# Kernel tuning notes

Measured on AMD Instinct MI355X. Metric: run time of the kernel, lower is better.

## Reference

```python
import jax, jax.numpy as jnp
import numpy as np

B, T, C = 4, 1024, 512      # batch, seq_len, n_attn
H, TT, D = 1, 1024, 16      # n_head (forced to 1 by kv.view), ctx_len, head_size


def setup_inputs() -> dict:
    key = jax.random.key(0)
    ks = jax.random.split(key, 13)
    s = 0.02
    return {
        "x": jax.random.normal(ks[0], (B, T, C), jnp.float32),
        "time_w": 1.0 + 0.1 * jax.random.normal(ks[1], (H, TT), jnp.float32),
        "time_alpha": 1.0 + 0.1 * jax.random.normal(ks[2], (H, 1, TT), jnp.float32),
        "time_beta": 1.0 + 0.1 * jax.random.normal(ks[3], (H, TT, 1), jnp.float32),
        "time_gamma": 1.0 + 0.1 * jax.random.normal(ks[4], (TT, 1), jnp.float32),
        "Wk": s * jax.random.normal(ks[5], (D, C), jnp.float32),
        "bk": jnp.zeros((D,), jnp.float32),
        "Wv": s * jax.random.normal(ks[6], (D, C), jnp.float32),
        "bv": jnp.zeros((D,), jnp.float32),
        "Wr": s * jax.random.normal(ks[7], (D, C), jnp.float32),
        "br": jnp.zeros((D,), jnp.float32),
        "Wo": s * jax.random.normal(ks[8], (64, D), jnp.float32),
        "bo": jnp.zeros((64,), jnp.float32),
    }


def reference(x, time_w, time_alpha, time_beta, time_gamma,
              Wk, bk, Wv, bv, Wr, br, Wo, bo):
    Tq = x.shape[1]
    # --- Toeplitz decay-matrix build (pad / tile / reshape trick) ---
    w = jnp.pad(time_w, ((0, 0), (0, TT)))                    # [H, 2TT]
    w = jnp.tile(w, (1, TT))[:, :-TT]                         # [H, 2TT*TT - TT]
    w = w.reshape(-1, TT, 2 * TT - 1)[:, :, TT - 1:]          # [H, TT, TT]
    w = w[:, :Tq, :Tq] * time_alpha[:, :, :Tq] * time_beta[:, :Tq, :]  # [H, T, T]
    # --- time shift on first half of channels (ZeroPad2d((0,0,1,-1))) ---
    half = x.shape[-1] // 2
    xs = jnp.pad(x[:, :, :half], ((0, 0), (1, 0), (0, 0)))[:, :-1]   # shift right by 1
    xx = jnp.concatenate([xs, x[:, :, half:]], axis=-1)              # [B, T, C]
    # --- k / v / r projections ---
    k = jnp.exp(jnp.clip(xx @ Wk.T + bk, -60.0, 30.0))        # [B, T, D]
    v = xx @ Wv.T + bv                                        # [B, T, D]
    r = xx @ Wr.T + br                                        # [B, T, D]
    sum_k = jnp.cumsum(k, axis=1)                             # [B, T, D]
    kv = k * v                                                # [B, T, D]
    # torch: kv.view(B,T,1,D).transpose(1,2) -> [B,1,T,D]; einsum 'htu,bthd->bhud'
    # broadcasts w's h=1 against kv's time axis and kv's t=1 against w's t axis:
    #   wkv[b,h,u,d] = (sum_t w[0,t,u]) * kv[b,h(time),d]
    w_sum = jnp.sum(w, axis=1)[0]                             # [T] over u
    wkv_full = w_sum[None, None, :, None] * kv[:, :, None, :] # [B, T, T, D]
    wkv = jnp.mean(wkv_full, axis=1)                          # mean over h -> [B, T, D]
    rwkv = r * wkv / (sum_k + 1e-8)                           # [B, T, D]
    out = (rwkv @ Wo.T + bo) * time_gamma[:Tq, :]             # [B, T, 64]
    return out
```

## Files before the change

### kernel.cpp

```cpp
#include <hip/hip_runtime.h>
#include <hip/hip_bf16.h>

typedef __hip_bfloat16 bf16;


__device__ __forceinline__ float ldf(const void* p, int f, long idx) {
    if (f == 0) return ((const float*)p)[idx];
    if (f == 1) {
        unsigned int u = ((unsigned int)((const unsigned short*)p)[idx]) << 16;
        float r; __builtin_memcpy(&r, &u, 4); return r;
    }
    return 0.f;
}

__device__ __forceinline__ int sniff_one(const unsigned short* u, int els) {
    int n16 = els < 64 ? els : 64;
    bool allzero = true;
    for (int j = 0; j < n16; ++j) if (u[j] != 0) { allzero = false; break; }
    if (allzero) return 2;
    int npair = n16 / 2;
    for (int j = 0; j < npair; ++j) {
        unsigned short lo = u[2 * j], hi = u[2 * j + 1];
        int elo = (lo >> 7) & 0xFF, ehi = (hi >> 7) & 0xFF;
        bool lo_ok = (elo >= 64 && elo <= 190) || lo == 0;
        bool hi_ok = (ehi >= 64 && ehi <= 190) || hi == 0;
        if (!(lo_ok && hi_ok)) return 0;
    }
    return 1;
}

__global__ __launch_bounds__(256) void setup_kernel(
    const void* x, const void* tw, const void* alpha, const void* beta,
    const void* gamma, const void* Wk, const void* bk, const void* Wv,
    const void* bv, const void* Wr, const void* br, const void* Wo,
    const void* bo,
    int n0, int n1, int n2, int n3, int n4, int n5, int n6, int n7,
    int n8, int n9, int n10, int n11, int n12,
    int* __restrict__ flags,
    float* __restrict__ WT4, float* __restrict__ biasWS,
    float* __restrict__ WoF, float* __restrict__ boF,
    float* __restrict__ gammaF, float* __restrict__ segzero,
    float* __restrict__ w_sum)
{
    __shared__ int sf[16];
    __shared__ float red[256];
    int tid = threadIdx.x;
    const void* ps[13] = {x,tw,alpha,beta,gamma,Wk,bk,Wv,bv,Wr,br,Wo,bo};
    int ns[13] = {n0,n1,n2,n3,n4,n5,n6,n7,n8,n9,n10,n11,n12};
    if (tid < 13) sf[tid] = sniff_one((const unsigned short*)ps[tid], ns[tid]);
    __syncthreads();
    if (blockIdx.x == 0 && tid < 14) {
        if (tid == 13) {
            int any16 = 0;
            for (int j = 0; j < 13; ++j) if (sf[j] == 1) any16 = 1;
            flags[13] = any16;
        } else {
            flags[tid] = sf[tid];
        }
    }

    int idx = blockIdx.x * 256 + tid;
    if (idx < 32768) {
        int q = idx >> 8, rem = idx & 255;
        int o = rem >> 2, c = q * 4 + (rem & 3);
        float val = 0.f;
        if (o < 16)      val = ldf(Wk, sf[5], (long)o * 512 + c);
        else if (o < 32) val = ldf(Wv, sf[7], (long)(o - 16) * 512 + c);
        else if (o < 48) val = ldf(Wr, sf[9], (long)(o - 32) * 512 + c);
        WT4[idx] = val;
    } else if (idx < 33792) {
        int i = idx - 32768;
        WoF[i] = ldf(Wo, sf[11], i);
    } else if (idx < 34816) {
        int i = idx - 33792;
        gammaF[i] = ldf(gamma, sf[4], i);
    } else if (idx < 34880) {
        int i = idx - 34816;
        boF[i] = ldf(bo, sf[12], i);
    } else if (idx < 34944) {
        int i = idx - 34880;
        float bb = 0.f;
        if (i < 16)      bb = ldf(bk, sf[6], i);
        else if (i < 32) bb = ldf(bv, sf[8], i - 16);
        else if (i < 48) bb = ldf(br, sf[10], i - 32);
        biasWS[i] = bb;
    } else if (idx < 36992) {
        segzero[idx - 34944] = 0.f;
    }

    int u = blockIdx.x;
    int ftw = sf[1], fal = sf[2], fbe = sf[3];
    float acc = 0.f;
    int n = 1024 - u;
    for (int s = tid; s < n; s += 256)
        acc += ldf(tw, ftw, 1023 - s) * ldf(beta, fbe, u + s);
    red[tid] = acc;
    __syncthreads();
    for (int off = 128; off > 0; off >>= 1) {
        if (tid < off) red[tid] += red[tid + off];
        __syncthreads();
    }
    if (tid == 0) w_sum[u] = red[0] * ldf(alpha, fal, u);
}

__global__ __launch_bounds__(256) void proj_kernel(
    const void* __restrict__ x, const float* __restrict__ WT4,
    const float* __restrict__ biasWS, const int* __restrict__ flg,
    float* __restrict__ k_ws, float* __restrict__ r_ws,
    float* __restrict__ segsum, float* __restrict__ segkv)
{
    __shared__ float xs[8 * 512];
    __shared__ float red[16 * 8 * 64];
    int tid = threadIdx.x;
    int row0 = blockIdx.x * 8;
    int b = row0 >> 10;
    int lt0 = row0 & 1023;
    int fx = flg[0];

    if (fx == 1) {
        const unsigned short* xp = (const unsigned short*)x;
        #pragma unroll
        for (int j = 0; j < 4; ++j) {
            int v = tid + 256 * j;
            int el = v * 4;
            int r = el >> 9, c = el & 511;
            int lt = lt0 + r - ((c < 256) ? 1 : 0);
            float4 f;
            if (lt < 0) f = make_float4(0.f, 0.f, 0.f, 0.f);
            else {
                const unsigned short* sp = xp + ((long)(b * 1024 + lt) * 512 + c);
                unsigned int u0 = ((unsigned int)sp[0]) << 16;
                unsigned int u1 = ((unsigned int)sp[1]) << 16;
                unsigned int u2 = ((unsigned int)sp[2]) << 16;
                unsigned int u3 = ((unsigned int)sp[3]) << 16;
                __builtin_memcpy(&f.x, &u0, 4); __builtin_memcpy(&f.y, &u1, 4);
                __builtin_memcpy(&f.z, &u2, 4); __builtin_memcpy(&f.w, &u3, 4);
            }
            reinterpret_cast<float4*>(xs)[v] = f;
        }
    } else {
        const float* xp = (const float*)x;
        #pragma unroll
        for (int j = 0; j < 4; ++j) {
            int v = tid + 256 * j;
            int el = v * 4;
            int r = el >> 9, c = el & 511;
            int lt = lt0 + r - ((c < 256) ? 1 : 0);
            float4 f;
            if (lt < 0) f = make_float4(0.f, 0.f, 0.f, 0.f);
            else f = *reinterpret_cast<const float4*>(xp + ((long)(b * 1024 + lt) * 512 + c));
            reinterpret_cast<float4*>(xs)[v] = f;
        }
    }
    __syncthreads();

    int o4 = tid & 15, cc = tid >> 4;
    const float4* xs4 = reinterpret_cast<const float4*>(xs);
    const float4* W4 = reinterpret_cast<const float4*>(WT4);
    float a0[8], a1[8], a2[8], a3[8];
    #pragma unroll
    for (int r = 0; r < 8; ++r) { a0[r] = a1[r] = a2[r] = a3[r] = 0.f; }
    #pragma unroll
    for (int q = 0; q < 8; ++q) {
        int cq = cc * 8 + q;
        float4 w0 = W4[cq * 64 + o4 * 4 + 0];
        float4 w1 = W4[cq * 64 + o4 * 4 + 1];
        float4 w2 = W4[cq * 64 + o4 * 4 + 2];
        float4 w3 = W4[cq * 64 + o4 * 4 + 3];
        #pragma unroll
        for (int r = 0; r < 8; ++r) {
            float4 x4 = xs4[r * 128 + cq];
            a0[r] += x4.x * w0.x + x4.y * w0.y + x4.z * w0.z + x4.w * w0.w;
            a1[r] += x4.x * w1.x + x4.y * w1.y + x4.z * w1.z + x4.w * w1.w;
            a2[r] += x4.x * w2.x + x4.y * w2.y + x4.z * w2.z + x4.w * w2.w;
            a3[r] += x4.x * w3.x + x4.y * w3.y + x4.z * w3.z + x4.w * w3.w;
        }
    }
    float4* red4 = reinterpret_cast<float4*>(red);
    #pragma unroll
    for (int r = 0; r < 8; ++r)
        red4[(cc * 8 + r) * 16 + o4] = make_float4(a0[r], a1[r], a2[r], a3[r]);
    __syncthreads();

    int seg = lt0 >> 6;
    #pragma unroll
    for (int it = 0; it < 2; ++it) {
        int idx = tid + 256 * it;
        int o2 = idx & 63, r2 = idx >> 6;
        float s = biasWS[o2];
        #pragma unroll
        for (int cc2 = 0; cc2 < 16; ++cc2)
            s += red[(cc2 * 8 + r2) * 64 + o2];
        long a = (long)(lt0 + r2) * 64 + b * 16 + (o2 & 15);
        if (o2 < 16) {
            k_ws[a] = expf(fminf(fmaxf(s, -60.f), 30.f));
        } else if (o2 < 32) {
            int d = o2 - 16;
            float sk = biasWS[d];
            #pragma unroll
            for (int cc2 = 0; cc2 < 16; ++cc2)
                sk += red[(cc2 * 8 + r2) * 64 + d];
            float kk = expf(fminf(fmaxf(sk, -60.f), 30.f));
            atomicAdd(&segsum[seg * 64 + b * 16 + d], kk);
            atomicAdd(&segkv[seg * 64 + b * 16 + d], kk * s);
        } else if (o2 < 48) {
            r_ws[a] = s;
        }
    }
}

__global__ __launch_bounds__(64) void scanC_kernel(
    float* k_ws, const float* __restrict__ segsum,
    const float* __restrict__ segkv, float* __restrict__ kvmean)
{
    int seg = blockIdx.x, bd = threadIdx.x;
    float run = 0.f;
    for (int s = 0; s < seg; ++s) run += segsum[s * 64 + bd];
    for (int i = 0; i < 64; ++i) {
        long a = (long)(seg * 64 + i) * 64 + bd;
        run += k_ws[a];
        k_ws[a] = run;
    }
    if (seg == 0) {
        float kvt = 0.f;
        for (int s = 0; s < 16; ++s) kvt += segkv[s * 64 + bd];
        kvmean[bd] = kvt * (1.0f / 1024.0f);
    }
}

__global__ __launch_bounds__(256) void out_kernel(
    const float* __restrict__ r_ws, const float* __restrict__ cumk,
    const float* __restrict__ kvmean, const float* __restrict__ w_sum,
    const float* __restrict__ WoF, const float* __restrict__ boF,
    const float* __restrict__ gammaF, const int* __restrict__ flg,
    void* __restrict__ out)
{
    int tid = threadIdx.x;
    int rl = tid >> 6, o = tid & 63;
    int row = blockIdx.x * 4 + rl;
    int b = row >> 10, t = row & 1023;
    __shared__ float rw[4][16];
    if (o < 16) {
        long a = (long)t * 64 + b * 16 + o;
        rw[rl][o] = r_ws[a] * w_sum[t] * kvmean[b * 16 + o] / (cumk[a] + 1e-8f);
    }
    __syncthreads();
    float acc = boF[o];
    const float4* W4 = reinterpret_cast<const float4*>(WoF + o * 16);
    #pragma unroll
    for (int j = 0; j < 4; ++j) {
        float4 w = W4[j];
        acc += rw[rl][4 * j + 0] * w.x + rw[rl][4 * j + 1] * w.y +
               rw[rl][4 * j + 2] * w.z + rw[rl][4 * j + 3] * w.w;
    }
    float val = acc * gammaF[t];
    if (flg[13]) ((bf16*)out)[(long)row * 64 + o] = __float2bfloat16(val);
    else         ((float*)out)[(long)row * 64 + o] = val;
}

extern "C" void kernel_launch(void* const* d_in, const int* in_sizes, int n_in,
                              void* d_out, int out_size, void* d_ws, size_t ws_size,
                              hipStream_t stream) {
    const void* x     = d_in[0];
    const void* tw    = d_in[1];
    const void* alpha = d_in[2];
    const void* beta  = d_in[3];
    const void* gamma = d_in[4];
    const void* Wk    = d_in[5];
    const void* bk    = d_in[6];
    const void* Wv    = d_in[7];
    const void* bv    = d_in[8];
    const void* Wr    = d_in[9];
    const void* br    = d_in[10];
    const void* Wo    = d_in[11];
    const void* bo    = d_in[12];

    float* ws     = (float*)d_ws;
    float* k_ws   = ws;
    float* r_ws   = ws + 65536;
    float* WT4    = ws + 131072;
    float* biasWS = ws + 163840;
    float* WoF    = ws + 163904;
    float* boF    = ws + 164928;
    float* gammaF = ws + 164992;
    float* kvmean = ws + 166016;
    float* w_sum  = ws + 166080;
    float* segsum = ws + 167104;
    float* segkv  = ws + 168128;
    int*   flags  = (int*)(ws + 169152);

    setup_kernel<<<1024, 256, 0, stream>>>(
        x, tw, alpha, beta, gamma, Wk, bk, Wv, bv, Wr, br, Wo, bo,
        in_sizes[0], in_sizes[1], in_sizes[2], in_sizes[3], in_sizes[4],
        in_sizes[5], in_sizes[6], in_sizes[7], in_sizes[8], in_sizes[9],
        in_sizes[10], in_sizes[11], in_sizes[12],
        flags, WT4, biasWS, WoF, boF, gammaF, segsum , w_sum);
    proj_kernel<<<512, 256, 0, stream>>>(x, WT4, biasWS, flags,
                                         k_ws, r_ws, segsum, segkv);
    scanC_kernel<<<16, 64, 0, stream>>>(k_ws, segsum, segkv, kvmean);
    out_kernel<<<1024, 256, 0, stream>>>(r_ws, k_ws, kvmean, w_sum,
                                         WoF, boF, gammaF, flags, (void*)d_out);
}
```

Before: 111.1 us.

## Fuse prefix-sum scan into output kernel and parallelize dtype sniffing

Removes the separate serial scan kernel that wrote cumulative k sums. Each output block now recomputes its own prefix sum from per-segment totals plus a partial in-segment reduction, and derives the kv mean from segkv directly. The per-input dtype sniffing in the setup kernel is spread across all threads with a warp shuffle and a shared atomic OR, replacing the per-thread serial loops. This saves a launch and a serial pass, but every output block now re-reads up to 64 rows of k plus the segment sums.

```diff
diff --git a/kernel.cpp b/kernel.cpp
--- a/kernel.cpp
+++ b/kernel.cpp
@@ -11,22 +11,6 @@
         float r; __builtin_memcpy(&r, &u, 4); return r;
     }
     return 0.f;
-}
-
-__device__ __forceinline__ int sniff_one(const unsigned short* u, int els) {
-    int n16 = els < 64 ? els : 64;
-    bool allzero = true;
-    for (int j = 0; j < n16; ++j) if (u[j] != 0) { allzero = false; break; }
-    if (allzero) return 2;
-    int npair = n16 / 2;
-    for (int j = 0; j < npair; ++j) {
-        unsigned short lo = u[2 * j], hi = u[2 * j + 1];
-        int elo = (lo >> 7) & 0xFF, ehi = (hi >> 7) & 0xFF;
-        bool lo_ok = (elo >= 64 && elo <= 190) || lo == 0;
-        bool hi_ok = (ehi >= 64 && ehi <= 190) || hi == 0;
-        if (!(lo_ok && hi_ok)) return 0;
-    }
-    return 1;
 }
 
 __global__ __launch_bounds__(256) void setup_kernel(
@@ -44,10 +28,45 @@
 {
     __shared__ int sf[16];
     __shared__ float red[256];
+    __shared__ unsigned mall;
     int tid = threadIdx.x;
     const void* ps[13] = {x,tw,alpha,beta,gamma,Wk,bk,Wv,bv,Wr,br,Wo,bo};
     int ns[13] = {n0,n1,n2,n3,n4,n5,n6,n7,n8,n9,n10,n11,n12};
-    if (tid < 13) sf[tid] = sniff_one((const unsigned short*)ps[tid], ns[tid]);
+
+    unsigned m = 0;
+    for (int t = tid; t < 13 * 64; t += 256) {
+        int p = t >> 6, j = t & 63;
+        int els = ns[p]; int n16 = els < 64 ? els : 64;
+        if (j < n16) {
+            unsigned short v = ((const unsigned short*)ps[p])[j];
+            if (v != 0) m |= (1u << p);
+        }
+    }
+    for (int t = tid; t < 13 * 32; t += 256) {
+        int p = t >> 5, jp = t & 31;
+        int els = ns[p]; int n16 = els < 64 ? els : 64; int npair = n16 >> 1;
+        if (jp < npair) {
+            const unsigned short* u = (const unsigned short*)ps[p];
+            unsigned short lo = u[2 * jp], hi = u[2 * jp + 1];
+            int elo = (lo >> 7) & 0xFF, ehi = (hi >> 7) & 0xFF;
+            bool lo_ok = (elo >= 64 && elo <= 190) || lo == 0;
+            bool hi_ok = (ehi >= 64 && ehi <= 190) || hi == 0;
+            if (!(lo_ok && hi_ok)) m |= (1u << (16 + p));
+        }
+    }
+    #pragma unroll
+    for (int off = 1; off < 64; off <<= 1) m |= __shfl_xor(m, off);
+    if (tid == 0) mall = 0;
+    __syncthreads();
+    if ((tid & 63) == 0) atomicOr(&mall, m);
+    __syncthreads();
+    unsigned mm = mall;
+    if (tid < 13) {
+        int f;
+        if (!((mm >> tid) & 1)) f = 2;
+        else f = ((mm >> (16 + tid)) & 1) ? 0 : 1;
+        sf[tid] = f;
+    }
     __syncthreads();
     if (blockIdx.x == 0 && tid < 14) {
         if (tid == 13) {
@@ -209,42 +228,63 @@
     }
 }
 
-__global__ __launch_bounds__(64) void scanC_kernel(
-    float* k_ws, const float* __restrict__ segsum,
-    const float* __restrict__ segkv, float* __restrict__ kvmean)
-{
-    int seg = blockIdx.x, bd = threadIdx.x;
-    float run = 0.f;
-    for (int s = 0; s < seg; ++s) run += segsum[s * 64 + bd];
-    for (int i = 0; i < 64; ++i) {
-        long a = (long)(seg * 64 + i) * 64 + bd;
-        run += k_ws[a];
-        k_ws[a] = run;
-    }
-    if (seg == 0) {
-        float kvt = 0.f;
-        for (int s = 0; s < 16; ++s) kvt += segkv[s * 64 + bd];
-        kvmean[bd] = kvt * (1.0f / 1024.0f);
-    }
-}
-
 __global__ __launch_bounds__(256) void out_kernel(
-    const float* __restrict__ r_ws, const float* __restrict__ cumk,
-    const float* __restrict__ kvmean, const float* __restrict__ w_sum,
-    const float* __restrict__ WoF, const float* __restrict__ boF,
-    const float* __restrict__ gammaF, const int* __restrict__ flg,
-    void* __restrict__ out)
+    const float* __restrict__ r_ws, const float* __restrict__ k_ws,
+    const float* __restrict__ segsum, const float* __restrict__ segkv,
+    const float* __restrict__ w_sum, const float* __restrict__ WoF,
+    const float* __restrict__ boF, const float* __restrict__ gammaF,
+    const int* __restrict__ flg, void* __restrict__ out)
 {
     int tid = threadIdx.x;
+    int row0 = blockIdx.x * 4;
+    int b = row0 >> 10;
+    int t0 = row0 & 1023;
+    int seg = (t0 + 3) >> 6;
+    int ncum = ((t0 + 3) & 63) + 1;
+    long base = (long)b * 16;
+    __shared__ float red2[256];
+    __shared__ float cum3[16], kvm[16], kk3[3][16];
+    __shared__ float rw[4][16];
+
+    int d = tid & 15, chunk = tid >> 4;
+    float p = 0.f;
+    for (int i = chunk; i < ncum; i += 16)
+        p += k_ws[(long)(seg * 64 + i) * 64 + base + d];
+    for (int s = chunk; s < seg; s += 16)
+        p += segsum[s * 64 + base + d];
+    red2[tid] = p;
+    __syncthreads();
+
+    if (tid < 16) {
+        float c = 0.f;
+        #pragma unroll
+        for (int ch = 0; ch < 16; ++ch) c += red2[ch * 16 + tid];
+        cum3[tid] = c;
+        float km = 0.f;
+        #pragma unroll
+        for (int s = 0; s < 16; ++s) km += segkv[s * 64 + base + tid];
+        kvm[tid] = km * (1.0f / 1024.0f);
+    } else if (tid < 64) {
+        int rr = (tid >> 4) - 1;
+        int dd = tid & 15;
+        kk3[rr][dd] = k_ws[(long)(t0 + 1 + rr) * 64 + base + dd];
+    }
+    __syncthreads();
+
+    if (tid < 64) {
+        int rl = tid >> 4, o = tid & 15;
+        float ck = cum3[o];
+        #pragma unroll
+        for (int j = 2; j >= 0; --j)
+            if (rl <= j) ck -= kk3[j][o];
+        int t = t0 + rl;
+        long a = (long)t * 64 + base + o;
+        rw[rl][o] = r_ws[a] * w_sum[t] * kvm[o] / (ck + 1e-8f);
+    }
+    __syncthreads();
+
     int rl = tid >> 6, o = tid & 63;
-    int row = blockIdx.x * 4 + rl;
-    int b = row >> 10, t = row & 1023;
-    __shared__ float rw[4][16];
-    if (o < 16) {
-        long a = (long)t * 64 + b * 16 + o;
-        rw[rl][o] = r_ws[a] * w_sum[t] * kvmean[b * 16 + o] / (cumk[a] + 1e-8f);
-    }
-    __syncthreads();
+    int t = t0 + rl;
     float acc = boF[o];
     const float4* W4 = reinterpret_cast<const float4*>(WoF + o * 16);
     #pragma unroll
@@ -254,8 +294,9 @@
                rw[rl][4 * j + 2] * w.z + rw[rl][4 * j + 3] * w.w;
     }
     float val = acc * gammaF[t];
-    if (flg[13]) ((bf16*)out)[(long)row * 64 + o] = __float2bfloat16(val);
-    else         ((float*)out)[(long)row * 64 + o] = val;
+    long oa = (long)(row0 + rl) * 64 + o;
+    if (flg[13]) ((bf16*)out)[oa] = __float2bfloat16(val);
+    else         ((float*)out)[oa] = val;
 }
 
 extern "C" void kernel_launch(void* const* d_in, const int* in_sizes, int n_in,
@@ -283,7 +324,6 @@
     float* WoF    = ws + 163904;
     float* boF    = ws + 164928;
     float* gammaF = ws + 164992;
-    float* kvmean = ws + 166016;
     float* w_sum  = ws + 166080;
     float* segsum = ws + 167104;
     float* segkv  = ws + 168128;
@@ -297,7 +337,6 @@
         flags, WT4, biasWS, WoF, boF, gammaF, segsum , w_sum);
     proj_kernel<<<512, 256, 0, stream>>>(x, WT4, biasWS, flags,
                                          k_ws, r_ws, segsum, segkv);
-    scanC_kernel<<<16, 64, 0, stream>>>(k_ws, segsum, segkv, kvmean);
-    out_kernel<<<1024, 256, 0, stream>>>(r_ws, k_ws, kvmean, w_sum,
+    out_kernel<<<1024, 256, 0, stream>>>(r_ws, k_ws, segsum, segkv, w_sum,
                                          WoF, boF, gammaF, flags, (void*)d_out);
 }
```

Result: faster. 102.3 us (-7.9%).
